# Kernel optimization log

Measured on AMD Instinct MI355X. Metric: run time of the kernel, lower is better.

## Reference

```python
import math
import jax, jax.numpy as jnp
import numpy as np
from jax import lax

B, C, O, K, WDIM, H, W = 8, 512, 512, 3, 512, 64, 64
CONV_SCALE = 1.0 / math.sqrt(C * K * K)
MOD_SCALE = 1.0 / math.sqrt(WDIM)


def setup_inputs() -> dict:
    key = jax.random.key(0)
    k1, k2, k3, k4 = jax.random.split(key, 4)
    return {
        "x": jax.random.normal(k1, (B, C, H, W), dtype=jnp.float32),
        "w": jax.random.normal(k2, (B, WDIM), dtype=jnp.float32),
        "base_weight": jax.random.normal(k3, (1, O, C, K, K), dtype=jnp.float32),
        "mod_weight": jax.random.normal(k4, (C, WDIM), dtype=jnp.float32),
        "mod_bias": jnp.zeros((C,), dtype=jnp.float32),
    }


def reference(x, w, base_weight, mod_weight, mod_bias):
    # EqualLinear modulation: s in (B, C), then +1
    s = w @ (mod_weight * MOD_SCALE).T + mod_bias + 1.0  # (B, C)
    # Per-sample modulated weights: (B, O, C, K, K)
    weight = CONV_SCALE * base_weight * s[:, None, :, None, None]
    # Demodulation
    d = lax.rsqrt(jnp.sum(weight * weight, axis=(2, 3, 4), keepdims=True))
    weight = weight * d
    pad = K // 2

    def conv_one(xi, wi):
        # xi: (C, H, W), wi: (O, C, K, K)
        return lax.conv_general_dilated(
            xi[None], wi, window_strides=(1, 1),
            padding=[(pad, pad), (pad, pad)],
            dimension_numbers=("NCHW", "OIHW", "NCHW"),
        )[0]

    return jax.vmap(conv_one)(x, weight)  # (B, O, H, W)
```

## Files before the change

kernel.cpp:

```cpp
#include <hip/hip_runtime.h>
#include <stdint.h>


#define MOD_SCALE  0.044194173824159216f
#define CONV_SCALE 0.014731391274719739f

typedef __attribute__((ext_vector_type(4))) float f32x4;
typedef __attribute__((ext_vector_type(8))) short bf16x8;

__device__ inline unsigned short f2bf(float f) {
  uint32_t u = __float_as_uint(f);
  uint32_t r = (u + 0x7fffu + ((u >> 16) & 1u)) >> 16;
  return (unsigned short)r;
}

__device__ inline void gload_lds16(const void* g, void* l) {
  __builtin_amdgcn_global_load_lds(
      (const __attribute__((address_space(1))) void*)g,
      (__attribute__((address_space(3))) void*)l, 16, 0, 0);
}

__global__ __launch_bounds__(256) void k_prep(const float* __restrict__ x,
                                              const float* __restrict__ w,
                                              const float* __restrict__ modw,
                                              const float* __restrict__ modb,
                                              unsigned short* __restrict__ xp,
                                              float* __restrict__ s_out) {
  __shared__ unsigned short smem[64 * 65];
  const int blk = blockIdx.x;
  const int tid = threadIdx.x;
  if (blk < 4096) {
    const int b = blk >> 9, r = blk & 511;
    const int c0 = ((r >> 6) << 6), p0 = ((r & 63) << 6);
    {
      const int pi = tid & 63, ci0 = tid >> 6;
      const float* src = x + (size_t)((b << 9) + c0 + ci0) * 4096 + p0 + pi;
#pragma unroll
      for (int it = 0; it < 16; ++it)
        smem[(ci0 + (it << 2)) * 65 + pi] = f2bf(src[(size_t)(it << 2) * 4096]);
    }
    __syncthreads();
    {
      const int cq = tid & 31, pq = tid >> 5;
#pragma unroll
      for (int it = 0; it < 8; ++it) {
        const int p = pq + (it << 3);
        const int gp = p0 + p;
        const int py = (gp >> 6) + 1, px = (gp & 63) + 1;
        uint32_t v = (uint32_t)smem[(cq << 1) * 65 + p] |
                     ((uint32_t)smem[((cq << 1) + 1) * 65 + p] << 16);
        ((uint32_t*)(xp + ((size_t)b * 4356 + py * 66 + px) * 512 + c0))[cq] = v;
      }
    }
  } else if (blk < 6176) {
    const int q = blk - 4096;
    const int b = q / 260, p = q - b * 260;
    int py, px;
    if (p < 66)       { py = 0;       px = p; }
    else if (p < 132) { py = 65;      px = p - 66; }
    else if (p < 196) { py = p - 131; px = 0; }
    else              { py = p - 195; px = 65; }
    uint32_t* dst = (uint32_t*)(xp + ((size_t)b * 4356 + py * 66 + px) * 512);
    dst[tid] = 0u;
  } else {
    float* red = (float*)smem;
    const int sb = blk - 6176;
    const int cb = sb & 7, b = sb >> 3;
    const int cl = tid >> 2, qq = tid & 3;
    const int c = (cb << 6) + cl;
    const float4* wd = (const float4*)(w + (b << 9) + (qq << 7));
    const float4* md = (const float4*)(modw + ((size_t)c << 9) + (qq << 7));
    float acc = 0.f;
#pragma unroll
    for (int i = 0; i < 32; ++i) {
      float4 a = wd[i], m = md[i];
      acc += a.x * m.x + a.y * m.y + a.z * m.z + a.w * m.w;
    }
    red[tid] = acc;
    __syncthreads();
    if (tid < 64) {
      float v = red[tid * 4] + red[tid * 4 + 1] + red[tid * 4 + 2] + red[tid * 4 + 3];
      int cc = (cb << 6) + tid;
      s_out[(b << 9) + cc] = v * MOD_SCALE + modb[cc] + 1.0f;
    }
  }
}

__global__ __launch_bounds__(256) void k_fw(const float* __restrict__ bw,
                                            const float* __restrict__ s,
                                            unsigned short* __restrict__ wm) {
  __shared__ float lw[4608];
  __shared__ float ls[4096];
  __shared__ float red[32];
  __shared__ float sc8[8];
  const int tid = threadIdx.x;
  const int o = blockIdx.x;
  {
    const float4* src = (const float4*)(bw + (size_t)o * 4608);
    float4* dst = (float4*)lw;
#pragma unroll
    for (int i = 0; i < 4; ++i) dst[tid + (i << 8)] = src[tid + (i << 8)];
    if (tid < 128) dst[tid + 1024] = src[tid + 1024];
  }
  {
    const float4* src = (const float4*)s;
    float4* dst = (float4*)ls;
#pragma unroll
    for (int i = 0; i < 4; ++i) dst[tid + (i << 8)] = src[tid + (i << 8)];
  }
  __syncthreads();
  const int c0 = tid << 1;
  const int base = c0 * 9;
  float wq0 = 0.f, wq1 = 0.f;
#pragma unroll
  for (int j = 0; j < 9; ++j) {
    float a = lw[base + j];      wq0 += a * a;
    float b2 = lw[base + 9 + j]; wq1 += b2 * b2;
  }
  const int lane = tid & 63, wv = tid >> 6;
#pragma unroll
  for (int b = 0; b < 8; ++b) {
    float s0 = ls[(b << 9) + c0], s1 = ls[(b << 9) + c0 + 1];
    float v = wq0 * s0 * s0 + wq1 * s1 * s1;
#pragma unroll
    for (int off = 32; off > 0; off >>= 1) v += __shfl_down(v, off, 64);
    if (lane == 0) red[(b << 2) + wv] = v;
  }
  __syncthreads();
  if (tid < 8) {
    float a = red[tid << 2] + red[(tid << 2) + 1] + red[(tid << 2) + 2] + red[(tid << 2) + 3];
    sc8[tid] = rsqrtf(a * (1.0f / 4608.0f)) * CONV_SCALE;
  }
  __syncthreads();
#pragma unroll 1
  for (int b = 0; b < 8; ++b) {
    const float dsc = sc8[b];
    const float s0 = ls[(b << 9) + c0] * dsc;
    const float s1 = ls[(b << 9) + c0 + 1] * dsc;
    uint32_t* dst = (uint32_t*)(wm + (size_t)((b << 9) + o) * 4608);
#pragma unroll
    for (int j = 0; j < 9; ++j) {
      float v0 = lw[base + j] * s0;
      float v1 = lw[base + 9 + j] * s1;
      dst[(j << 8) + tid] = (uint32_t)f2bf(v0) | ((uint32_t)f2bf(v1) << 16);
    }
  }
}

__global__ __launch_bounds__(256, 2) void k_conv(const unsigned short* __restrict__ wmodT,
                                                 const unsigned short* __restrict__ xpad,
                                                 float* __restrict__ out) {
  __shared__ alignas(16) unsigned short As[3 * 8192];
  __shared__ alignas(16) unsigned short Bs[8448];
  const int tid = threadIdx.x;
  const int b  = blockIdx.z;
  const int m0 = blockIdx.y << 7;
  const int n0 = blockIdx.x << 7;
  const int y0 = n0 >> 6;

  const int srow = tid >> 3;
  const int schk = ((tid & 7) - (srow & 7)) & 7;
  const int scol = schk << 3;

  const unsigned short* A0 = wmodT + (size_t)((b << 9) + m0 + srow) * 4608 + scol;
  const size_t bx = (size_t)b * (66 * 66 * 512);

  const int lane = tid & 63;
  const int wv   = tid >> 6;
  const int moff = (wv >> 1) << 6;
  const int noff = (wv & 1) << 6;
  const int noffp = noff ? 66 : 0;
  const int lm   = lane & 15;
  const int g4   = lane >> 4;

  const unsigned short* ardA[2];
#pragma unroll
  for (int h = 0; h < 2; ++h)
    ardA[h] = As + (moff + lm) * 64 + ((((h << 2) + g4) + moff + lm) & 7) * 8;
  const unsigned short* ardB[3][2];
#pragma unroll
  for (int kx = 0; kx < 3; ++kx) {
    const int rb = noffp + lm + kx;
#pragma unroll
    for (int h = 0; h < 2; ++h)
      ardB[kx][h] = Bs + rb * 64 + ((((h << 2) + g4) + rb) & 7) * 8;
  }

  f32x4 acc[4][4];
#pragma unroll
  for (int i = 0; i < 4; ++i)
#pragma unroll
    for (int j = 0; j < 4; ++j) acc[i][j] = (f32x4){0.f, 0.f, 0.f, 0.f};

#pragma unroll 1
  for (int ky = 0; ky < 3; ++ky) {
    const unsigned short* Bp0 = xpad + bx + (size_t)((y0 + ky) * 66 + srow) * 512 + scol;
#pragma unroll 1
    for (int kb = 0; kb < 8; ++kb) {
      const int kcol = kb << 6;
#pragma unroll
      for (int kx = 0; kx < 3; ++kx) {
        const unsigned short* Ap = A0 + ((ky * 3 + kx) << 9) + kcol;
#pragma unroll
        for (int g = 0; g < 4; ++g)
          gload_lds16(Ap + g * (32 * 4608), As + ((kx << 13) + (((g << 8) + tid) << 3)));
      }
      const unsigned short* Bp = Bp0 + kcol;
#pragma unroll
      for (int g = 0; g < 4; ++g)
        gload_lds16(Bp + g * (32 * 512), Bs + (((g << 8) + tid) << 3));
      if (tid < 32) gload_lds16(Bp + 128 * 512, Bs + 8192 + tid * 8);
      __syncthreads();
#pragma unroll
      for (int kx = 0; kx < 3; ++kx) {
#pragma unroll
        for (int h = 0; h < 2; ++h) {
          bf16x8 af[4], bf[4];
          const unsigned short* pa = ardA[h] + (kx << 13);
          const unsigned short* pb = ardB[kx][h];
#pragma unroll
          for (int i = 0; i < 4; ++i) af[i] = *(const bf16x8*)(pa + (i << 10));
#pragma unroll
          for (int j = 0; j < 4; ++j) bf[j] = *(const bf16x8*)(pb + (j << 10));
#pragma unroll
          for (int i = 0; i < 4; ++i)
#pragma unroll
            for (int j = 0; j < 4; ++j)
              acc[i][j] = __builtin_amdgcn_mfma_f32_16x16x32_bf16(af[i], bf[j], acc[i][j], 0, 0, 0);
        }
      }
      __syncthreads();
    }
  }

  float* op = out + (size_t)((b << 9) + m0 + moff) * 4096 + n0 + noff;
#pragma unroll
  for (int i = 0; i < 4; ++i) {
#pragma unroll
    for (int r = 0; r < 4; ++r) {
      const int m = i * 16 + (g4 << 2) + r;
#pragma unroll
      for (int j = 0; j < 4; ++j)
        op[(size_t)m * 4096 + (j << 4) + lm] = acc[i][j][r];
    }
  }
}

extern "C" void kernel_launch(void* const* d_in, const int* in_sizes, int n_in,
                              void* d_out, int out_size, void* d_ws, size_t ws_size,
                              hipStream_t stream) {
  const float* x    = (const float*)d_in[0];
  const float* w    = (const float*)d_in[1];
  const float* bw   = (const float*)d_in[2];
  const float* modw = (const float*)d_in[3];
  const float* modb = (const float*)d_in[4];
  float* out = (float*)d_out;
  char* ws = (char*)d_ws;

  float* s_buf = (float*)(ws);
  unsigned short* wmod = (unsigned short*)(ws + 16384);
  unsigned short* xpad = (unsigned short*)(ws + 37765120);

  (void)in_sizes; (void)n_in; (void)out_size; (void)ws_size;

  k_prep<<<6240, 256, 0, stream>>>(x, w, modw, modb, xpad, s_buf);
  k_fw  <<<512, 256, 0, stream>>>(bw, s_buf, wmod);
  k_conv<<<dim3(32, 4, 8), 256, 0, stream>>>(wmod, xpad, out);
}
```

Baseline: 270.3 us.

## Fold style modulation into input and demodulation into conv epilogue

Instead of building a per-sample modulated weight tensor (B×O×C×9 bf16), the style scale s is applied to the input activations during padding/conversion and the demodulation factor is applied per output channel in the conv epilogue. A single shared bf16 weight tensor is produced and reused by all batch samples. This removes the write and reread of about 37 MB of per-sample weights and improves L2 reuse of A tiles across batches. The cost is one extra kernel launch for the style GEMV and a multiply per output, with slightly different bf16 rounding because x*s is quantized instead of w*s.

Result: faster. 261.5 us (-3.3%).

```diff
diff --git a/kernel.cpp b/kernel.cpp
--- a/kernel.cpp
+++ b/kernel.cpp
@@ -20,12 +20,36 @@
       (__attribute__((address_space(3))) void*)l, 16, 0, 0);
 }
 
+__global__ __launch_bounds__(256) void k_style(const float* __restrict__ w,
+                                               const float* __restrict__ modw,
+                                               const float* __restrict__ modb,
+                                               float* __restrict__ s_out) {
+  __shared__ float red[256];
+  const int tid = threadIdx.x;
+  const int sb = blockIdx.x;
+  const int cb = sb & 7, b = sb >> 3;
+  const int cl = tid >> 2, qq = tid & 3;
+  const int c = (cb << 6) + cl;
+  const float4* wd = (const float4*)(w + (b << 9) + (qq << 7));
+  const float4* md = (const float4*)(modw + ((size_t)c << 9) + (qq << 7));
+  float acc = 0.f;
+#pragma unroll
+  for (int i = 0; i < 32; ++i) {
+    float4 a = wd[i], m = md[i];
+    acc += a.x * m.x + a.y * m.y + a.z * m.z + a.w * m.w;
+  }
+  red[tid] = acc;
+  __syncthreads();
+  if (tid < 64) {
+    float v = red[tid * 4] + red[tid * 4 + 1] + red[tid * 4 + 2] + red[tid * 4 + 3];
+    int cc = (cb << 6) + tid;
+    s_out[(b << 9) + cc] = v * MOD_SCALE + modb[cc] + 1.0f;
+  }
+}
+
 __global__ __launch_bounds__(256) void k_prep(const float* __restrict__ x,
-                                              const float* __restrict__ w,
-                                              const float* __restrict__ modw,
-                                              const float* __restrict__ modb,
-                                              unsigned short* __restrict__ xp,
-                                              float* __restrict__ s_out) {
+                                              const float* __restrict__ s,
+                                              unsigned short* __restrict__ xp) {
   __shared__ unsigned short smem[64 * 65];
   const int blk = blockIdx.x;
   const int tid = threadIdx.x;
@@ -35,9 +59,11 @@
     {
       const int pi = tid & 63, ci0 = tid >> 6;
       const float* src = x + (size_t)((b << 9) + c0 + ci0) * 4096 + p0 + pi;
+      const float* sv = s + (b << 9) + c0 + ci0;
 #pragma unroll
       for (int it = 0; it < 16; ++it)
-        smem[(ci0 + (it << 2)) * 65 + pi] = f2bf(src[(size_t)(it << 2) * 4096]);
+        smem[(ci0 + (it << 2)) * 65 + pi] =
+            f2bf(src[(size_t)(it << 2) * 4096] * sv[it << 2]);
     }
     __syncthreads();
     {
@@ -52,7 +78,7 @@
         ((uint32_t*)(xp + ((size_t)b * 4356 + py * 66 + px) * 512 + c0))[cq] = v;
       }
     }
-  } else if (blk < 6176) {
+  } else {
     const int q = blk - 4096;
     const int b = q / 260, p = q - b * 260;
     int py, px;
@@ -62,37 +88,16 @@
     else              { py = p - 195; px = 65; }
     uint32_t* dst = (uint32_t*)(xp + ((size_t)b * 4356 + py * 66 + px) * 512);
     dst[tid] = 0u;
-  } else {
-    float* red = (float*)smem;
-    const int sb = blk - 6176;
-    const int cb = sb & 7, b = sb >> 3;
-    const int cl = tid >> 2, qq = tid & 3;
-    const int c = (cb << 6) + cl;
-    const float4* wd = (const float4*)(w + (b << 9) + (qq << 7));
-    const float4* md = (const float4*)(modw + ((size_t)c << 9) + (qq << 7));
-    float acc = 0.f;
-#pragma unroll
-    for (int i = 0; i < 32; ++i) {
-      float4 a = wd[i], m = md[i];
-      acc += a.x * m.x + a.y * m.y + a.z * m.z + a.w * m.w;
-    }
-    red[tid] = acc;
-    __syncthreads();
-    if (tid < 64) {
-      float v = red[tid * 4] + red[tid * 4 + 1] + red[tid * 4 + 2] + red[tid * 4 + 3];
-      int cc = (cb << 6) + tid;
-      s_out[(b << 9) + cc] = v * MOD_SCALE + modb[cc] + 1.0f;
-    }
-  }
-}
-
-__global__ __launch_bounds__(256) void k_fw(const float* __restrict__ bw,
-                                            const float* __restrict__ s,
-                                            unsigned short* __restrict__ wm) {
+  }
+}
+
+__global__ __launch_bounds__(256) void k_fwd(const float* __restrict__ bw,
+                                             const float* __restrict__ s,
+                                             unsigned short* __restrict__ awT,
+                                             float* __restrict__ d_out) {
   __shared__ float lw[4608];
   __shared__ float ls[4096];
   __shared__ float red[32];
-  __shared__ float sc8[8];
   const int tid = threadIdx.x;
   const int o = blockIdx.x;
   {
@@ -129,26 +134,18 @@
   __syncthreads();
   if (tid < 8) {
     float a = red[tid << 2] + red[(tid << 2) + 1] + red[(tid << 2) + 2] + red[(tid << 2) + 3];
-    sc8[tid] = rsqrtf(a * (1.0f / 4608.0f)) * CONV_SCALE;
-  }
-  __syncthreads();
-#pragma unroll 1
-  for (int b = 0; b < 8; ++b) {
-    const float dsc = sc8[b];
-    const float s0 = ls[(b << 9) + c0] * dsc;
-    const float s1 = ls[(b << 9) + c0 + 1] * dsc;
-    uint32_t* dst = (uint32_t*)(wm + (size_t)((b << 9) + o) * 4608);
-#pragma unroll
-    for (int j = 0; j < 9; ++j) {
-      float v0 = lw[base + j] * s0;
-      float v1 = lw[base + 9 + j] * s1;
-      dst[(j << 8) + tid] = (uint32_t)f2bf(v0) | ((uint32_t)f2bf(v1) << 16);
-    }
-  }
-}
-
-__global__ __launch_bounds__(256, 2) void k_conv(const unsigned short* __restrict__ wmodT,
+    d_out[(tid << 9) + o] = rsqrtf(a * (1.0f / 4608.0f)) * CONV_SCALE;
+  }
+  uint32_t* dst = (uint32_t*)(awT + (size_t)o * 4608);
+#pragma unroll
+  for (int j = 0; j < 9; ++j)
+    dst[(j << 8) + tid] = (uint32_t)f2bf(lw[base + j]) |
+                          ((uint32_t)f2bf(lw[base + 9 + j]) << 16);
+}
+
+__global__ __launch_bounds__(256, 2) void k_conv(const unsigned short* __restrict__ awT,
                                                  const unsigned short* __restrict__ xpad,
+                                                 const float* __restrict__ dmod,
                                                  float* __restrict__ out) {
   __shared__ alignas(16) unsigned short As[3 * 8192];
   __shared__ alignas(16) unsigned short Bs[8448];
@@ -162,7 +159,7 @@
   const int schk = ((tid & 7) - (srow & 7)) & 7;
   const int scol = schk << 3;
 
-  const unsigned short* A0 = wmodT + (size_t)((b << 9) + m0 + srow) * 4608 + scol;
+  const unsigned short* A0 = awT + (size_t)(m0 + srow) * 4608 + scol;
   const size_t bx = (size_t)b * (66 * 66 * 512);
 
   const int lane = tid & 63;
@@ -233,15 +230,17 @@
     }
   }
 
+  const float* dB = dmod + (b << 9) + m0 + moff;
   float* op = out + (size_t)((b << 9) + m0 + moff) * 4096 + n0 + noff;
 #pragma unroll
   for (int i = 0; i < 4; ++i) {
 #pragma unroll
     for (int r = 0; r < 4; ++r) {
       const int m = i * 16 + (g4 << 2) + r;
+      const float dm = dB[m];
 #pragma unroll
       for (int j = 0; j < 4; ++j)
-        op[(size_t)m * 4096 + (j << 4) + lm] = acc[i][j][r];
+        op[(size_t)m * 4096 + (j << 4) + lm] = acc[i][j][r] * dm;
     }
   }
 }
@@ -258,12 +257,14 @@
   char* ws = (char*)d_ws;
 
   float* s_buf = (float*)(ws);
-  unsigned short* wmod = (unsigned short*)(ws + 16384);
-  unsigned short* xpad = (unsigned short*)(ws + 37765120);
+  float* d_buf = (float*)(ws + 16384);
+  unsigned short* awT  = (unsigned short*)(ws + 32768);
+  unsigned short* xpad = (unsigned short*)(ws + 4751360);
 
   (void)in_sizes; (void)n_in; (void)out_size; (void)ws_size;
 
-  k_prep<<<6240, 256, 0, stream>>>(x, w, modw, modb, xpad, s_buf);
-  k_fw  <<<512, 256, 0, stream>>>(bw, s_buf, wmod);
-  k_conv<<<dim3(32, 4, 8), 256, 0, stream>>>(wmod, xpad, out);
-}
+  k_style<<<64,   256, 0, stream>>>(w, modw, modb, s_buf);
+  k_prep <<<6176, 256, 0, stream>>>(x, s_buf, xpad);
+  k_fwd  <<<512,  256, 0, stream>>>(bw, s_buf, awT, d_buf);
+  k_conv <<<dim3(32, 4, 8), 256, 0, stream>>>(awT, xpad, d_buf, out);
+}
```
